# Kernel optimization log

Measured on AMD Instinct MI355X. Metric: run time of the kernel, lower is better.

The kernel has to match this reference:

```python
import jax, jax.numpy as jnp
import numpy as np

N, D, H, C, E = 16384, 768, 768, 2, 20

def setup_inputs() -> dict:
    key = jax.random.key(0)
    k1, k2, k3, k4, k5, k6 = jax.random.split(key, 6)
    return {
        "embeddings": jax.random.normal(k1, (N, D), dtype=jnp.float32),
        "component_idx": jax.random.randint(k2, (N,), 0, E, dtype=jnp.int64),
        "W1": jax.random.normal(k3, (E, D, H), dtype=jnp.float32) * (1.0 / np.sqrt(D)),
        "b1": jnp.zeros((E, H), dtype=jnp.float32),
        "W2": jax.random.normal(k4, (E, H, C), dtype=jnp.float32) * (1.0 / np.sqrt(H)),
        "b2": jnp.zeros((E, C), dtype=jnp.float32),
    }

def reference(embeddings, component_idx, W1, b1, W2, b2):
    # Each token n goes through expert component_idx[n]:
    #   y = relu(x @ W1[e] + b1[e]) @ W2[e] + b2[e]
    # The torch module's mask/cat/argsort reassembly is mathematically a
    # per-token select of its own expert's output at the original position.
    # Dense-expert formulation (standard jax MoE fallback), then gather.
    h = jax.nn.relu(jnp.einsum('nd,edh->enh', embeddings, W1) + b1[:, None, :])  # [E,N,H]
    y = jnp.einsum('enh,ehc->enc', h, W2) + b2[:, None, :]                        # [E,N,C]
    n_idx = jnp.arange(embeddings.shape[0])
    return y[component_idx, n_idx]  # [N,C]
```

## Files before the change

### kernel.cpp

```cpp
#include <hip/hip_runtime.h>

#define N_D 768
#define N_H 768
#define N_C 2
#define N_E 20
#define MT 128
#define NT 128
#define BK 32
#define MAX_TILES 160

typedef __attribute__((ext_vector_type(8))) short short8;
typedef __attribute__((ext_vector_type(4))) float f32x4;

__device__ __forceinline__ unsigned short f2bf(float f) {
  unsigned u = __builtin_bit_cast(unsigned, f);
  u += 0x7FFFu + ((u >> 16) & 1u);
  return (unsigned short)(u >> 16);
}

#define GLD_LDS16(gp, lp)                                                        \
  __builtin_amdgcn_global_load_lds(                                              \
      (const __attribute__((address_space(1))) void*)(gp),                       \
      (__attribute__((address_space(3))) void*)(lp), 16, 0, 0)


__global__ __launch_bounds__(256) void k_hist(const int* __restrict__ cidx,
                                              int* __restrict__ counts, int n) {
  __shared__ int lc[N_E];
  if (threadIdx.x < N_E) lc[threadIdx.x] = 0;
  __syncthreads();
  for (int i = blockIdx.x * blockDim.x + threadIdx.x; i < n;
       i += gridDim.x * blockDim.x) {
    int e = cidx[i];
    e = e < 0 ? 0 : (e >= N_E ? N_E - 1 : e);
    atomicAdd(&lc[e], 1);
  }
  __syncthreads();
  if (threadIdx.x < N_E) atomicAdd(&counts[threadIdx.x], lc[threadIdx.x]);
}

__global__ void k_scan(const int* __restrict__ counts, int* __restrict__ offsets,
                       int* __restrict__ cursor, int* __restrict__ tiles,
                       int* __restrict__ numTiles) {
  if (threadIdx.x == 0) {
    int run = 0, t = 0;
    for (int e = 0; e < N_E; ++e) {
      offsets[e] = run;
      cursor[e] = run;
      int nt = (counts[e] + MT - 1) / MT;
      for (int m = 0; m < nt && t < MAX_TILES; ++m) tiles[t++] = (e << 8) | m;
      run += counts[e];
    }
    *numTiles = t;
  }
}

__global__ __launch_bounds__(256) void k_scatter(const int* __restrict__ cidx,
                                                 int* __restrict__ cursor,
                                                 int* __restrict__ sorted, int n) {
  __shared__ int lc[N_E];
  __shared__ int lbase[N_E];
  int tid = threadIdx.x;
  if (tid < N_E) lc[tid] = 0;
  __syncthreads();
  int i = blockIdx.x * blockDim.x + tid;
  int e = 0, p = 0;
  if (i < n) {
    e = cidx[i];
    e = e < 0 ? 0 : (e >= N_E ? N_E - 1 : e);
    p = atomicAdd(&lc[e], 1);
  }
  __syncthreads();
  if (tid < N_E) lbase[tid] = atomicAdd(&cursor[tid], lc[tid]);
  __syncthreads();
  if (i < n) sorted[lbase[e] + p] = i;
}


__global__ __launch_bounds__(192) void k_gather(const float* __restrict__ emb,
                                                const int* __restrict__ sorted,
                                                unsigned short* __restrict__ Xg,
                                                int n) {
  int row = blockIdx.x;
  int j = threadIdx.x;
  ushort4 o;
  if (row < n) {
    float4 v = ((const float4*)(emb + (size_t)sorted[row] * N_D))[j];
    o.x = f2bf(v.x);
    o.y = f2bf(v.y);
    o.z = f2bf(v.z);
    o.w = f2bf(v.w);
  } else {
    o.x = o.y = o.z = o.w = 0;
  }
  ((ushort4*)(Xg + (size_t)row * N_D))[j] = o;
}


__global__ __launch_bounds__(256) void k_w1_cvt(const float* __restrict__ W1,
                                                unsigned short* __restrict__ W1t) {
  __shared__ float tile[64][65];
  int e = blockIdx.z, h0 = blockIdx.x * 64, d0 = blockIdx.y * 64;
  const float* src = W1 + (size_t)e * N_D * N_H;
  unsigned short* dst = W1t + (size_t)e * N_H * N_D;
  int tx = threadIdx.x & 15, ty = threadIdx.x >> 4;
  for (int s = 0; s < 4; ++s) {
    int d = s * 16 + ty;
    float4 v = *(const float4*)&src[(size_t)(d0 + d) * N_H + h0 + tx * 4];
    tile[d][tx * 4 + 0] = v.x;
    tile[d][tx * 4 + 1] = v.y;
    tile[d][tx * 4 + 2] = v.z;
    tile[d][tx * 4 + 3] = v.w;
  }
  __syncthreads();
  for (int s = 0; s < 4; ++s) {
    int h = s * 16 + ty;
    ushort4 o;
    o.x = f2bf(tile[tx * 4 + 0][h]);
    o.y = f2bf(tile[tx * 4 + 1][h]);
    o.z = f2bf(tile[tx * 4 + 2][h]);
    o.w = f2bf(tile[tx * 4 + 3][h]);
    *(ushort4*)&dst[(size_t)(h0 + h) * N_D + d0 + tx * 4] = o;
  }
}


__global__ __launch_bounds__(256, 2) void k_gemm(
    const unsigned short* __restrict__ Xg, const unsigned short* __restrict__ W1t,
    const float* __restrict__ b1, const float* __restrict__ W2,
    const float* __restrict__ b2, const int* __restrict__ sorted,
    const int* __restrict__ counts, const int* __restrict__ offsets,
    const int* __restrict__ tiles, const int* __restrict__ numTiles,
    float* __restrict__ out) {
  if ((int)blockIdx.y >= *numTiles) return;
  const int tv = tiles[blockIdx.y];
  const int e = tv >> 8;
  const int m0 = (tv & 255) * MT;
  const int off = offsets[e];
  const int cnt_rel = counts[e] - m0;
  const int n0 = blockIdx.x * NT;

  __shared__ unsigned short lA[MT * BK];
  __shared__ unsigned short lB[NT * BK];

  const int tid = threadIdx.x;
  const int wid = tid >> 6, lane = tid & 63;
  const int wm = (wid >> 1) * 64, wn = (wid & 1) * 64;
  const int quad = lane >> 4, lm = lane & 15;

  const unsigned short* ag =
      Xg + (size_t)(off + m0 + wid * 32 + (lane >> 2)) * N_D + (lane & 3) * 8;
  const unsigned short* bg = W1t + (size_t)e * N_H * N_D +
                             (size_t)(n0 + wid * 32 + (lane >> 2)) * N_D +
                             (lane & 3) * 8;

  f32x4 acc[4][4] = {};

  for (int kt = 0; kt < N_D / BK; ++kt) {
    __syncthreads();
    const unsigned short* agk = ag + kt * BK;
    const unsigned short* bgk = bg + kt * BK;
    GLD_LDS16(agk, &lA[(wid * 32) * BK]);
    GLD_LDS16(agk + 16 * N_D, &lA[(wid * 32 + 16) * BK]);
    GLD_LDS16(bgk, &lB[(wid * 32) * BK]);
    GLD_LDS16(bgk + 16 * N_D, &lB[(wid * 32 + 16) * BK]);
    __syncthreads();

    short8 af[4], bfr[4];
    for (int i = 0; i < 4; ++i)
      af[i] = *(const short8*)&lA[(wm + i * 16 + lm) * BK + quad * 8];
    for (int j = 0; j < 4; ++j)
      bfr[j] = *(const short8*)&lB[(wn + j * 16 + lm) * BK + quad * 8];
    for (int i = 0; i < 4; ++i)
      for (int j = 0; j < 4; ++j)
        acc[i][j] =
            __builtin_amdgcn_mfma_f32_16x16x32_bf16(af[i], bfr[j], acc[i][j], 0, 0, 0);
  }

  float y0[4][4], y1[4][4];
  for (int i = 0; i < 4; ++i)
    for (int r = 0; r < 4; ++r) y0[i][r] = y1[i][r] = 0.f;

  for (int j = 0; j < 4; ++j) {
    int col = n0 + wn + j * 16 + lm;
    float bias = b1[e * N_H + col];
    float2 w2 = *(const float2*)&W2[((size_t)e * N_H + col) * N_C];
    for (int i = 0; i < 4; ++i) {
      f32x4 a = acc[i][j];
      for (int r = 0; r < 4; ++r) {
        float h = a[r] + bias;
        h = h > 0.f ? h : 0.f;
        y0[i][r] += h * w2.x;
        y1[i][r] += h * w2.y;
      }
    }
  }
  for (int s = 1; s < 16; s <<= 1) {
    for (int i = 0; i < 4; ++i)
      for (int r = 0; r < 4; ++r) {
        y0[i][r] += __shfl_xor(y0[i][r], s, 64);
        y1[i][r] += __shfl_xor(y1[i][r], s, 64);
      }
  }
  if (lm == 0) {
    const bool add_bias = (n0 == 0) && (wn == 0);
    float bb0 = add_bias ? b2[e * N_C + 0] : 0.f;
    float bb1 = add_bias ? b2[e * N_C + 1] : 0.f;
    for (int i = 0; i < 4; ++i) {
      for (int r = 0; r < 4; ++r) {
        int mrel = wm + i * 16 + quad * 4 + r;
        if (mrel < cnt_rel) {
          int token = sorted[off + m0 + mrel];
          atomicAdd(&out[(size_t)token * N_C + 0], y0[i][r] + bb0);
          atomicAdd(&out[(size_t)token * N_C + 1], y1[i][r] + bb1);
        }
      }
    }
  }
}


extern "C" void kernel_launch(void* const* d_in, const int* in_sizes, int n_in,
                              void* d_out, int out_size, void* d_ws, size_t ws_size,
                              hipStream_t stream) {
  const float* emb = (const float*)d_in[0];
  const int* cidx = (const int*)d_in[1];
  const float* W1 = (const float*)d_in[2];
  const float* b1 = (const float*)d_in[3];
  const float* W2 = (const float*)d_in[4];
  const float* b2 = (const float*)d_in[5];
  float* out = (float*)d_out;
  const int n = in_sizes[1];

  char* ws = (char*)d_ws;
  int* counts = (int*)ws;
  int* offsets = (int*)(ws + 128);
  int* cursor = (int*)(ws + 256);
  int* numTiles = (int*)(ws + 384);
  int* tiles = (int*)(ws + 512);
  int* sorted = (int*)(ws + 2048);
  size_t sorted_bytes = ((size_t)n * 4 + 255) & ~(size_t)255;
  unsigned short* Xg = (unsigned short*)(ws + 2048 + sorted_bytes);
  int pcap = n + MT;
  unsigned short* W1t = Xg + (size_t)pcap * N_D;

  hipMemsetAsync(d_ws, 0, 2048, stream);
  hipMemsetAsync(d_out, 0, (size_t)out_size * sizeof(float), stream);
  int nb = (n + 255) / 256;
  k_hist<<<nb, 256, 0, stream>>>(cidx, counts, n);
  k_scan<<<1, 64, 0, stream>>>(counts, offsets, cursor, tiles, numTiles);
  k_scatter<<<nb, 256, 0, stream>>>(cidx, cursor, sorted, n);
  k_gather<<<pcap, 192, 0, stream>>>(emb, sorted, Xg, n);
  k_w1_cvt<<<dim3(N_H / 64, N_D / 64, N_E), 256, 0, stream>>>(W1, W1t);
  k_gemm<<<dim3(N_H / NT, MAX_TILES), 256, 0, stream>>>(
      Xg, W1t, b1, W2, b2, sorted, counts, offsets, tiles, numTiles, out);
}
```

Measured before the change: 224.0 us.

## Double-buffer LDS tiles with XOR swizzle in expert GEMM and widen W1 stores

```diff
diff --git a/kernel.cpp b/kernel.cpp
--- a/kernel.cpp
+++ b/kernel.cpp
@@ -7,6 +7,7 @@
 #define MT 128
 #define NT 128
 #define BK 32
+#define KT (N_D / BK)
 #define MAX_TILES 160
 
 typedef __attribute__((ext_vector_type(8))) short short8;
@@ -113,14 +114,13 @@
     tile[d][tx * 4 + 3] = v.w;
   }
   __syncthreads();
-  for (int s = 0; s < 4; ++s) {
-    int h = s * 16 + ty;
-    ushort4 o;
-    o.x = f2bf(tile[tx * 4 + 0][h]);
-    o.y = f2bf(tile[tx * 4 + 1][h]);
-    o.z = f2bf(tile[tx * 4 + 2][h]);
-    o.w = f2bf(tile[tx * 4 + 3][h]);
-    *(ushort4*)&dst[(size_t)(h0 + h) * N_D + d0 + tx * 4] = o;
+  int px = threadIdx.x & 7, py = threadIdx.x >> 3;
+  for (int s = 0; s < 2; ++s) {
+    int h = s * 32 + py;
+    short8 v;
+    for (int j = 0; j < 8; ++j)
+      v[j] = (short)f2bf(tile[px * 8 + j][h]);
+    *(short8*)&dst[(size_t)(h0 + h) * N_D + d0 + px * 8] = v;
   }
 }
 
@@ -140,37 +140,54 @@
   const int cnt_rel = counts[e] - m0;
   const int n0 = blockIdx.x * NT;
 
-  __shared__ unsigned short lA[MT * BK];
-  __shared__ unsigned short lB[NT * BK];
+  __shared__ unsigned short lA[2][MT * BK];
+  __shared__ unsigned short lB[2][NT * BK];
 
   const int tid = threadIdx.x;
   const int wid = tid >> 6, lane = tid & 63;
   const int wm = (wid >> 1) * 64, wn = (wid & 1) * 64;
   const int quad = lane >> 4, lm = lane & 15;
 
+  const int srow = lane >> 2;
+  const int schunk = (lane & 3) ^ (srow & 3);
   const unsigned short* ag =
-      Xg + (size_t)(off + m0 + wid * 32 + (lane >> 2)) * N_D + (lane & 3) * 8;
+      Xg + (size_t)(off + m0 + wid * 32 + srow) * N_D + schunk * 8;
   const unsigned short* bg = W1t + (size_t)e * N_H * N_D +
-                             (size_t)(n0 + wid * 32 + (lane >> 2)) * N_D +
-                             (lane & 3) * 8;
+                             (size_t)(n0 + wid * 32 + srow) * N_D + schunk * 8;
+  unsigned short* lAw0 = &lA[0][(wid * 32) * BK];
+  unsigned short* lAw1 = &lA[1][(wid * 32) * BK];
+  unsigned short* lBw0 = &lB[0][(wid * 32) * BK];
+  unsigned short* lBw1 = &lB[1][(wid * 32) * BK];
+
+  const int koff = (quad ^ (lm & 3)) * 8;
 
   f32x4 acc[4][4] = {};
 
-  for (int kt = 0; kt < N_D / BK; ++kt) {
+  {
+    GLD_LDS16(ag, lAw0);
+    GLD_LDS16(ag + 16 * N_D, lAw0 + 16 * BK);
+    GLD_LDS16(bg, lBw0);
+    GLD_LDS16(bg + 16 * N_D, lBw0 + 16 * BK);
+  }
+
+  for (int kt = 0; kt < KT; ++kt) {
+    const int cur = kt & 1;
     __syncthreads();
-    const unsigned short* agk = ag + kt * BK;
-    const unsigned short* bgk = bg + kt * BK;
-    GLD_LDS16(agk, &lA[(wid * 32) * BK]);
-    GLD_LDS16(agk + 16 * N_D, &lA[(wid * 32 + 16) * BK]);
-    GLD_LDS16(bgk, &lB[(wid * 32) * BK]);
-    GLD_LDS16(bgk + 16 * N_D, &lB[(wid * 32 + 16) * BK]);
-    __syncthreads();
-
+    if (kt + 1 < KT) {
+      const unsigned short* agk = ag + (kt + 1) * BK;
+      const unsigned short* bgk = bg + (kt + 1) * BK;
+      unsigned short* la = cur ? lAw0 : lAw1;
+      unsigned short* lb = cur ? lBw0 : lBw1;
+      GLD_LDS16(agk, la);
+      GLD_LDS16(agk + 16 * N_D, la + 16 * BK);
+      GLD_LDS16(bgk, lb);
+      GLD_LDS16(bgk + 16 * N_D, lb + 16 * BK);
+    }
     short8 af[4], bfr[4];
     for (int i = 0; i < 4; ++i)
-      af[i] = *(const short8*)&lA[(wm + i * 16 + lm) * BK + quad * 8];
+      af[i] = *(const short8*)&lA[cur][(wm + i * 16 + lm) * BK + koff];
     for (int j = 0; j < 4; ++j)
-      bfr[j] = *(const short8*)&lB[(wn + j * 16 + lm) * BK + quad * 8];
+      bfr[j] = *(const short8*)&lB[cur][(wn + j * 16 + lm) * BK + koff];
     for (int i = 0; i < 4; ++i)
       for (int j = 0; j < 4; ++j)
         acc[i][j] =
```

New measurement: 223.5 us. About the same (-0.2%).
